# Kernel tuning notes

Measured on AMD Instinct MI355X. Metric: run time of the kernel, lower is better.

## Reference

```python
import jax, jax.numpy as jnp
import numpy as np

N_HEAD = 32
N_KV_HEAD = 8
HEAD_DIM = 64
ROPE_BASE = 10000.0


def _rope_tables(T, dim):
    inv_freq = 1.0 / (ROPE_BASE ** (jnp.arange(0, dim, 2, dtype=jnp.float32) / dim))
    t = jnp.arange(T, dtype=jnp.float32)
    freqs = jnp.outer(t, inv_freq)            # [T, dim/2]
    emb = jnp.concatenate([freqs, freqs], -1)  # [T, dim]
    return jnp.cos(emb), jnp.sin(emb)


def _rotate_half(x):
    x1, x2 = jnp.split(x, 2, axis=-1)
    return jnp.concatenate([-x2, x1], axis=-1)


def setup_inputs() -> dict:
    key = jax.random.key(0)
    ks = jax.random.split(key, 5)
    B, T, C = 2, 2048, 2048
    kv_dim = N_KV_HEAD * HEAD_DIM
    s = 0.02
    return {
        "x":  jax.random.normal(ks[0], (B, T, C), jnp.float32),
        "Wq": jax.random.normal(ks[1], (C, C), jnp.float32) * s,
        "Wk": jax.random.normal(ks[2], (C, kv_dim), jnp.float32) * s,
        "Wv": jax.random.normal(ks[3], (C, kv_dim), jnp.float32) * s,
        "Wo": jax.random.normal(ks[4], (C, C), jnp.float32) * s,
    }


def reference(x, Wq, Wk, Wv, Wo):
    B, T, C = x.shape
    n_rep = N_HEAD // N_KV_HEAD  # 4 query heads per KV head

    q = (x @ Wq).reshape(B, T, N_HEAD, HEAD_DIM).transpose(0, 2, 1, 3)      # [B,H,T,d]
    k = (x @ Wk).reshape(B, T, N_KV_HEAD, HEAD_DIM).transpose(0, 2, 1, 3)   # [B,Hk,T,d]
    v = (x @ Wv).reshape(B, T, N_KV_HEAD, HEAD_DIM).transpose(0, 2, 1, 3)   # [B,Hk,T,d]

    cos, sin = _rope_tables(T, HEAD_DIM)  # [T,d], broadcast over batch/heads
    q = q * cos + _rotate_half(q) * sin
    k = k * cos + _rotate_half(k) * sin

    # group Q heads by their shared KV head (equivalent to repeat_interleave on K/V)
    qg = q.reshape(B, N_KV_HEAD, n_rep, T, HEAD_DIM)
    scale = 1.0 / np.sqrt(HEAD_DIM).astype(np.float32)
    att = jnp.einsum('bgrtd,bgsd->bgrts', qg, k) * scale  # [B,Hk,rep,T,T]

    causal = jnp.tril(jnp.ones((T, T), dtype=bool))
    att = jnp.where(causal, att, -jnp.inf)
    att = jax.nn.softmax(att, axis=-1)

    y = jnp.einsum('bgrts,bgsd->bgrtd', att, v)            # [B,Hk,rep,T,d]
    y = y.reshape(B, N_HEAD, T, HEAD_DIM).transpose(0, 2, 1, 3).reshape(B, T, C)
    return y @ Wo
```

## Files before the change

### kernel.cpp

```cpp
#include <hip/hip_runtime.h>
#include <hip/hip_bf16.h>
#include <math.h>

#define B_SZ    2
#define T_SEQ   2048
#define C_DIM   2048
#define N_HEAD  32
#define N_KVH   8
#define HDIM    64
#define KV_DIM  (N_KVH * HDIM)
#define M_ROWS  (B_SZ * T_SEQ)
#define RLN     0.28782313662425575f

typedef __bf16 bf16x8 __attribute__((ext_vector_type(8)));
typedef float f32x4 __attribute__((ext_vector_type(4)));
typedef unsigned short u16x4 __attribute__((ext_vector_type(4)));
typedef unsigned short u16x8 __attribute__((ext_vector_type(8)));

__device__ inline unsigned short f2bf(float f) {
    __bf16 h = (__bf16)f;
    return __builtin_bit_cast(unsigned short, h);
}


__global__ __launch_bounds__(256) void convert_a(const float* __restrict__ A,
                                                 unsigned short* __restrict__ Ab,
                                                 int K) {
    const int G = blockIdx.x * 256 + threadIdx.x;
    const int t = G >> 10;
    const int w = G & 1023;
    const int g = w & 7, m = w >> 3;
    const int KT = K >> 6;
    const int mh = t / KT, kt = t % KT;
    const float* src = A + (size_t)(mh * 128 + m) * K + kt * 64 + g * 8;
    const float4 a = *(const float4*)src;
    const float4 b = *(const float4*)(src + 4);
    u16x8 o;
    o[0] = f2bf(a.x); o[1] = f2bf(a.y); o[2] = f2bf(a.z); o[3] = f2bf(a.w);
    o[4] = f2bf(b.x); o[5] = f2bf(b.y); o[6] = f2bf(b.z); o[7] = f2bf(b.w);
    *(u16x8*)(Ab + (size_t)t * 8192 + g * 1024 + m * 8) = o;
}

__global__ __launch_bounds__(256) void convert_w(const float* __restrict__ W,
                                                 unsigned short* __restrict__ Wb,
                                                 int K, int N) {
    const int G = blockIdx.x * 256 + threadIdx.x;
    const int t = G >> 10;
    const int w = G & 1023;
    const int n = w & 127, g = w >> 7;
    const int KT = K >> 6;
    const int nh = t / KT, kt = t % KT;
    const float* src = W + (size_t)(kt * 64 + g * 8) * N + nh * 128 + n;
    u16x8 o;
    #pragma unroll
    for (int j = 0; j < 8; ++j) o[j] = f2bf(src[(size_t)j * N]);
    *(u16x8*)(Wb + (size_t)t * 8192 + g * 1024 + n * 8) = o;
}

#define G_LDS16(SRC, DST)                                                      \
    __builtin_amdgcn_global_load_lds(                                          \
        (const __attribute__((address_space(1))) unsigned int*)(SRC),          \
        (__attribute__((address_space(3))) unsigned int*)(DST), 16, 0, 0)

#define STAGE(GB, LB)                                                          \
    do {                                                                       \
        G_LDS16((GB) + ch * 512 + lane * 8, (LB) + ch * 512);                  \
        G_LDS16((GB) + (ch + 1) * 512 + lane * 8, (LB) + (ch + 1) * 512);      \
    } while (0)

#define MFMA16(AF, IB, JB)                                                     \
    _Pragma("unroll")                                                          \
    for (int i_ = 0; i_ < 4; ++i_)                                             \
        _Pragma("unroll")                                                      \
        for (int j_ = 0; j_ < 2; ++j_) {                                       \
            acc[(IB) + i_][(JB) + j_] = __builtin_amdgcn_mfma_f32_16x16x32_bf16( \
                AF[i_][0], bfr[(JB) + j_][0], acc[(IB) + i_][(JB) + j_], 0, 0, 0); \
            acc[(IB) + i_][(JB) + j_] = __builtin_amdgcn_mfma_f32_16x16x32_bf16( \
                AF[i_][1], bfr[(JB) + j_][1], acc[(IB) + i_][(JB) + j_], 0, 0, 0); \
        }

__device__ __forceinline__ void gemm256_core(const unsigned short* __restrict__ Ab,
                                             const unsigned short* __restrict__ Bb,
                                             const int K, f32x4 (&acc)[8][4]) {
    __shared__ __align__(16) unsigned short lds[2][4][8192];

    const int tid  = threadIdx.x;
    const int wave = tid >> 6, lane = tid & 63;
    const int quad = lane >> 4, l15 = lane & 15;
    const int wm = wave >> 2, wn = wave & 3;
    const int NT = K >> 6;
    const unsigned short* At = Ab + (size_t)(blockIdx.y * 2) * NT * 8192;
    const unsigned short* Bt = Bb + (size_t)(blockIdx.x * 2) * NT * 8192;
    const int ch = wave * 2;

    const int abase = quad * 1024 + l15 * 8;
    const int bbase = quad * 1024 + ((wn & 1) * 64 + l15) * 8;

    #pragma unroll
    for (int i = 0; i < 8; ++i)
        #pragma unroll
        for (int j = 0; j < 4; ++j) acc[i][j] = (f32x4){0.f, 0.f, 0.f, 0.f};

    STAGE(At,                              lds[0][0]);
    STAGE(At + (size_t)NT * 8192,          lds[0][1]);
    STAGE(Bt,                              lds[0][2]);
    STAGE(Bt + (size_t)NT * 8192,          lds[0][3]);
    STAGE(At + 8192,                       lds[1][0]);
    STAGE(At + (size_t)NT * 8192 + 8192,   lds[1][1]);
    asm volatile("s_waitcnt vmcnt(4)" ::: "memory");
    __builtin_amdgcn_s_barrier();

    for (int t = 0; t < NT; ++t) {
        unsigned short (*L)[8192]  = lds[t & 1];
        unsigned short (*Ln)[8192] = lds[(t & 1) ^ 1];
        const unsigned short* Abuf = L[wm];
        const unsigned short* Bbuf = L[2 + (wn >> 1)];
        bf16x8 af0[4][2], af1[4][2], bfr[4][2];

        #pragma unroll
        for (int i = 0; i < 4; ++i) {
            af0[i][0] = *(const bf16x8*)(Abuf + abase + i * 128);
            af0[i][1] = *(const bf16x8*)(Abuf + abase + 4096 + i * 128);
        }
        #pragma unroll
        for (int j = 0; j < 2; ++j) {
            bfr[j][0] = *(const bf16x8*)(Bbuf + bbase + j * 128);
            bfr[j][1] = *(const bf16x8*)(Bbuf + bbase + 4096 + j * 128);
        }
        if (t + 1 < NT) STAGE(Bt + (size_t)(t + 1) * 8192, Ln[2]);
        asm volatile("s_waitcnt lgkmcnt(8)" ::: "memory");
        __builtin_amdgcn_s_barrier();
        asm volatile("s_waitcnt lgkmcnt(0)" ::: "memory");
        __builtin_amdgcn_sched_barrier(0);
        __builtin_amdgcn_s_setprio(1);
        MFMA16(af0, 0, 0)
        __builtin_amdgcn_s_setprio(0);
        __builtin_amdgcn_sched_barrier(0);
        __builtin_amdgcn_s_barrier();

        #pragma unroll
        for (int i = 0; i < 4; ++i) {
            af1[i][0] = *(const bf16x8*)(Abuf + abase + (4 + i) * 128);
            af1[i][1] = *(const bf16x8*)(Abuf + abase + 4096 + (4 + i) * 128);
        }
        #pragma unroll
        for (int j = 0; j < 2; ++j) {
            bfr[2 + j][0] = *(const bf16x8*)(Bbuf + bbase + (2 + j) * 128);
            bfr[2 + j][1] = *(const bf16x8*)(Bbuf + bbase + 4096 + (2 + j) * 128);
        }
        if (t + 1 < NT) STAGE(Bt + (size_t)(NT + t + 1) * 8192, Ln[3]);
        asm volatile("s_waitcnt lgkmcnt(8)" ::: "memory");
        __builtin_amdgcn_s_barrier();
        asm volatile("s_waitcnt lgkmcnt(0)" ::: "memory");
        __builtin_amdgcn_sched_barrier(0);
        __builtin_amdgcn_s_setprio(1);
        MFMA16(af1, 4, 0)
        __builtin_amdgcn_s_setprio(0);
        __builtin_amdgcn_sched_barrier(0);
        __builtin_amdgcn_s_barrier();

        if (t + 2 < NT) STAGE(At + (size_t)(t + 2) * 8192, L[0]);
        __builtin_amdgcn_s_barrier();
        __builtin_amdgcn_sched_barrier(0);
        __builtin_amdgcn_s_setprio(1);
        MFMA16(af0, 0, 2)
        __builtin_amdgcn_s_setprio(0);
        __builtin_amdgcn_sched_barrier(0);
        __builtin_amdgcn_s_barrier();

        if (t + 2 < NT) {
            STAGE(At + (size_t)(NT + t + 2) * 8192, L[1]);
            asm volatile("s_waitcnt vmcnt(4)" ::: "memory");
        } else {
            asm volatile("s_waitcnt vmcnt(0)" ::: "memory");
        }
        __builtin_amdgcn_s_barrier();
        __builtin_amdgcn_sched_barrier(0);
        __builtin_amdgcn_s_setprio(1);
        MFMA16(af1, 4, 2)
        __builtin_amdgcn_s_setprio(0);
        __builtin_amdgcn_sched_barrier(0);
        __builtin_amdgcn_s_barrier();
    }
}

__global__ __launch_bounds__(512, 2) void gemm256(const unsigned short* __restrict__ Ab,
                                                  const unsigned short* __restrict__ Bb,
                                                  float* __restrict__ C,
                                                  int N, int K) {
    f32x4 acc[8][4];
    gemm256_core(Ab, Bb, K, acc);
    const int tid  = threadIdx.x;
    const int wave = tid >> 6, lane = tid & 63;
    const int quad = lane >> 4, l15 = lane & 15;
    const int wm = wave >> 2, wn = wave & 3;
    const int row0 = blockIdx.y * 256 + wm * 128 + quad * 4;
    const int col0 = blockIdx.x * 256 + wn * 64 + l15;
    #pragma unroll
    for (int i = 0; i < 8; ++i)
        #pragma unroll
        for (int r = 0; r < 4; ++r) {
            const int row = row0 + i * 16 + r;
            #pragma unroll
            for (int j = 0; j < 4; ++j)
                C[(size_t)row * N + col0 + j * 16] = acc[i][j][r];
        }
}

__global__ __launch_bounds__(512, 2) void gemm256_qkv(const unsigned short* __restrict__ Ab,
                                                      const unsigned short* __restrict__ Bb,
                                                      unsigned short* __restrict__ Qb,
                                                      unsigned short* __restrict__ Kbuf,
                                                      unsigned short* __restrict__ Vt,
                                                      int K) {
    f32x4 acc[8][4];
    gemm256_core(Ab, Bb, K, acc);
    const int tid  = threadIdx.x;
    const int wave = tid >> 6, lane = tid & 63;
    const int quad = lane >> 4, l15 = lane & 15;
    const int wm = wave >> 2, wn = wave & 3;
    const int cb = blockIdx.x * 256 + wn * 64;
    const int m0 = blockIdx.y * 256 + wm * 128 + quad * 4;

    if (cb < 2048) {
        const int h = cb >> 6;
        const float invf0 = __expf(-(float)l15 * RLN);
        const float invf1 = __expf(-(float)(l15 + 16) * RLN);
        #pragma unroll
        for (int i = 0; i < 8; ++i)
            #pragma unroll
            for (int r = 0; r < 4; ++r) {
                const int row = m0 + i * 16 + r;
                const float t = (float)(row & (T_SEQ - 1));
                float s0, c0, s1, c1;
                sincosf(t * invf0, &s0, &c0);
                sincosf(t * invf1, &s1, &c1);
                const float x0 = acc[i][0][r], x1 = acc[i][1][r];
                const float x2 = acc[i][2][r], x3 = acc[i][3][r];
                unsigned short* dst = Qb + (size_t)row * C_DIM + h * HDIM + l15;
                dst[0]  = f2bf((x0 * c0 - x2 * s0) * 0.125f);
                dst[16] = f2bf((x1 * c1 - x3 * s1) * 0.125f);
                dst[32] = f2bf((x2 * c0 + x0 * s0) * 0.125f);
                dst[48] = f2bf((x3 * c1 + x1 * s1) * 0.125f);
            }
    } else if (cb < 2560) {
        const int kvh = (cb - 2048) >> 6;
        const float invf0 = __expf(-(float)l15 * RLN);
        const float invf1 = __expf(-(float)(l15 + 16) * RLN);
        const int c8l = l15 >> 3, dil = l15 & 7;
        #pragma unroll
        for (int i = 0; i < 8; ++i)
            #pragma unroll
            for (int r = 0; r < 4; ++r) {
                const int row = m0 + i * 16 + r;
                const int tt = row & (T_SEQ - 1);
                const int bb = row >> 11;
                const float t = (float)tt;
                float s0, c0, s1, c1;
                sincosf(t * invf0, &s0, &c0);
                sincosf(t * invf1, &s1, &c1);
                const float x0 = acc[i][0][r], x1 = acc[i][1][r];
                const float x2 = acc[i][2][r], x3 = acc[i][3][r];
                unsigned short* dst = Kbuf + (size_t)((bb * N_KVH + kvh) * 32 + (tt >> 6)) * 4096;
                const int kk = tt & 63;
                dst[((c8l + 0) * 64 + kk) * 8 + dil] = f2bf(x0 * c0 - x2 * s0);
                dst[((c8l + 2) * 64 + kk) * 8 + dil] = f2bf(x1 * c1 - x3 * s1);
                dst[((c8l + 4) * 64 + kk) * 8 + dil] = f2bf(x2 * c0 + x0 * s0);
                dst[((c8l + 6) * 64 + kk) * 8 + dil] = f2bf(x3 * c1 + x1 * s1);
            }
    } else {
        const int kvh = (cb - 2560) >> 6;
        const int bb = m0 >> 11;
        #pragma unroll
        for (int i = 0; i < 8; ++i) {
            const int t0 = (m0 + i * 16) & (T_SEQ - 1);
            const int o = (t0 >> 3) & 7, i8 = t0 & 7;
            unsigned short* dst = Vt + (size_t)((bb * N_KVH + kvh) * 32 + (t0 >> 6)) * 4096;
            #pragma unroll
            for (int j = 0; j < 4; ++j) {
                const int d = j * 16 + l15;
                u16x4 pk;
                pk[0] = f2bf(acc[i][j][0]); pk[1] = f2bf(acc[i][j][1]);
                pk[2] = f2bf(acc[i][j][2]); pk[3] = f2bf(acc[i][j][3]);
                *(u16x4*)(dst + (o * 64 + d) * 8 + i8) = pk;
            }
        }
    }
}

__global__ __launch_bounds__(256, 2) void attn_mfma(const unsigned short* __restrict__ Qb,
                                                    const unsigned short* __restrict__ Kbuf,
                                                    const unsigned short* __restrict__ Vt,
                                                    unsigned short* __restrict__ Yb) {
    __shared__ __align__(16) unsigned short Ps[4][1152];

    const int bid = blockIdx.x;
    const int x   = bid & 7;
    const int g   = bid >> 3;
    const int combo = x * 2 + (g & 1);
    const int qc  = 31 - (g >> 1);
    const int b   = combo >> 3;
    const int kvh = combo & 7;

    const int tid  = threadIdx.x;
    const int wave = tid >> 6, lane = tid & 63;
    const int quad = lane >> 4, l15 = lane & 15;
    const int h    = kvh * 4 + wave;
    const int qw   = qc * 64;

    bf16x8 qf[4][2];
    #pragma unroll
    for (int mt = 0; mt < 4; ++mt) {
        const size_t qoff = (size_t)(b * T_SEQ + qw + mt * 16 + l15) * C_DIM + h * HDIM + quad * 8;
        qf[mt][0] = *(const bf16x8*)(Qb + qoff);
        qf[mt][1] = *(const bf16x8*)(Qb + qoff + 32);
    }

    const unsigned short* kbase = Kbuf + (size_t)((b * N_KVH + kvh) * 32) * 4096;
    const unsigned short* vbase = Vt + (size_t)((b * N_KVH + kvh) * 32) * 4096;

    f32x4 acc[4][4];
    #pragma unroll
    for (int mt = 0; mt < 4; ++mt)
        #pragma unroll
        for (int c = 0; c < 4; ++c) acc[mt][c] = (f32x4){0.f, 0.f, 0.f, 0.f};
    float psum[4][4];
    #pragma unroll
    for (int mt = 0; mt < 4; ++mt)
        #pragma unroll
        for (int r = 0; r < 4; ++r) psum[mt][r] = 0.f;

    for (int jt = 0; jt <= qc; ++jt) {
        const unsigned short* kt = kbase + (size_t)jt * 4096;
        const unsigned short* vt = vbase + (size_t)jt * 4096;

        bf16x8 kf[4][2], vf[2][4];
        #pragma unroll
        for (int st = 0; st < 4; ++st)
            #pragma unroll
            for (int c = 0; c < 2; ++c)
                kf[st][c] = *(const bf16x8*)&kt[((c * 4 + quad) * 64 + l15 * 4 + st) * 8];
        #pragma unroll
        for (int kc = 0; kc < 2; ++kc)
            #pragma unroll
            for (int c = 0; c < 4; ++c)
                vf[kc][c] = *(const bf16x8*)&vt[((kc * 4 + quad) * 64 + c * 16 + l15) * 8];

        const bool diag = (jt == qc);
        const int j0 = jt << 6;

        #pragma unroll
        for (int mt = 0; mt < 4; ++mt) {
            f32x4 sacc[4];
            #pragma unroll
            for (int st = 0; st < 4; ++st) {
                f32x4 s = (f32x4){0.f, 0.f, 0.f, 0.f};
                s = __builtin_amdgcn_mfma_f32_16x16x32_bf16(qf[mt][0], kf[st][0], s, 0, 0, 0);
                s = __builtin_amdgcn_mfma_f32_16x16x32_bf16(qf[mt][1], kf[st][1], s, 0, 0, 0);
                sacc[st] = s;
            }

            float p[4][4];
            if (!diag) {
                #pragma unroll
                for (int st = 0; st < 4; ++st)
                    #pragma unroll
                    for (int r = 0; r < 4; ++r)
                        p[st][r] = __expf(sacc[st][r]);
            } else {
                #pragma unroll
                for (int st = 0; st < 4; ++st)
                    #pragma unroll
                    for (int r = 0; r < 4; ++r) {
                        const int key = j0 + l15 * 4 + st;
                        const int q   = qw + mt * 16 + quad * 4 + r;
                        p[st][r] = __expf(key > q ? -1e30f : sacc[st][r]);
                    }
            }
            #pragma unroll
            for (int r = 0; r < 4; ++r) {
                u16x4 pk;
                pk[0] = f2bf(p[0][r]); pk[1] = f2bf(p[1][r]);
                pk[2] = f2bf(p[2][r]); pk[3] = f2bf(p[3][r]);
                *(u16x4*)&Ps[wave][(quad * 4 + r) * 72 + l15 * 4] = pk;
                psum[mt][r] += (p[0][r] + p[1][r]) + (p[2][r] + p[3][r]);
            }

            #pragma unroll
            for (int kc = 0; kc < 2; ++kc) {
                const bf16x8 pa = *(const bf16x8*)&Ps[wave][l15 * 72 + kc * 32 + quad * 8];
                #pragma unroll
                for (int c = 0; c < 4; ++c)
                    acc[mt][c] = __builtin_amdgcn_mfma_f32_16x16x32_bf16(pa, vf[kc][c], acc[mt][c], 0, 0, 0);
            }
        }
    }

    #pragma unroll
    for (int mt = 0; mt < 4; ++mt)
        #pragma unroll
        for (int r = 0; r < 4; ++r) {
            float s = psum[mt][r];
            #pragma unroll
            for (int off = 1; off < 16; off <<= 1) s += __shfl_xor(s, off, 16);
            const float inv = 1.0f / s;
            const int grow = b * T_SEQ + qw + mt * 16 + quad * 4 + r;
            const int mh = grow >> 7, m = grow & 127;
            #pragma unroll
            for (int c = 0; c < 4; ++c) {
                const int gk = c * 2 + (l15 >> 3);
                Yb[(size_t)(mh * 32 + h) * 8192 + gk * 1024 + m * 8 + (l15 & 7)]
                    = f2bf(acc[mt][c][r] * inv);
            }
        }
}

extern "C" void kernel_launch(void* const* d_in, const int* in_sizes, int n_in,
                              void* d_out, int out_size, void* d_ws, size_t ws_size,
                              hipStream_t stream) {
    const float* x  = (const float*)d_in[0];
    const float* Wq = (const float*)d_in[1];
    const float* Wk = (const float*)d_in[2];
    const float* Wv = (const float*)d_in[3];
    const float* Wo = (const float*)d_in[4];

    char* base = (char*)d_ws;
    unsigned short* xb    = (unsigned short*)(base + 0);
    unsigned short* Wqkvb = (unsigned short*)(base + (16ull << 20));
    unsigned short* Wob   = (unsigned short*)(base + (28ull << 20));
    unsigned short* Qb    = (unsigned short*)(base + (36ull << 20));
    unsigned short* Kb    = (unsigned short*)(base + (52ull << 20));
    unsigned short* Vt    = (unsigned short*)(base + (56ull << 20));
    unsigned short* Yb    = xb;

    const dim3 blk(256);

    convert_a<<<(M_ROWS * C_DIM) / 2048, blk, 0, stream>>>(x, xb, C_DIM);
    convert_w<<<(C_DIM * C_DIM) / 2048, blk, 0, stream>>>(Wq, Wqkvb, C_DIM, C_DIM);
    convert_w<<<(C_DIM * KV_DIM) / 2048, blk, 0, stream>>>(Wk, Wqkvb + (size_t)16 * 32 * 8192, C_DIM, KV_DIM);
    convert_w<<<(C_DIM * KV_DIM) / 2048, blk, 0, stream>>>(Wv, Wqkvb + (size_t)20 * 32 * 8192, C_DIM, KV_DIM);
    convert_w<<<(C_DIM * C_DIM) / 2048, blk, 0, stream>>>(Wo, Wob, C_DIM, C_DIM);

    gemm256_qkv<<<dim3(3072 / 256, M_ROWS / 256), dim3(512), 0, stream>>>(xb, Wqkvb, Qb, Kb, Vt, C_DIM);

    attn_mfma<<<B_SZ * N_KVH * (T_SEQ / 64), blk, 0, stream>>>(Qb, Kb, Vt, Yb);

    gemm256<<<dim3(C_DIM / 256, M_ROWS / 256), dim3(512), 0, stream>>>(Yb, Wob, (float*)d_out, C_DIM, C_DIM);
}
```

Baseline: 331.2 us.

## Reorder GEMM phases to reuse A fragments and cut fragment registers

```diff
diff --git a/kernel.cpp b/kernel.cpp
--- a/kernel.cpp
+++ b/kernel.cpp
@@ -68,16 +68,41 @@
         G_LDS16((GB) + (ch + 1) * 512 + lane * 8, (LB) + (ch + 1) * 512);      \
     } while (0)
 
-#define MFMA16(AF, IB, JB)                                                     \
+#define MFMA16(IB, JB)                                                         \
     _Pragma("unroll")                                                          \
     for (int i_ = 0; i_ < 4; ++i_)                                             \
         _Pragma("unroll")                                                      \
         for (int j_ = 0; j_ < 2; ++j_) {                                       \
             acc[(IB) + i_][(JB) + j_] = __builtin_amdgcn_mfma_f32_16x16x32_bf16( \
-                AF[i_][0], bfr[(JB) + j_][0], acc[(IB) + i_][(JB) + j_], 0, 0, 0); \
+                af[i_][0], bf[j_][0], acc[(IB) + i_][(JB) + j_], 0, 0, 0);     \
             acc[(IB) + i_][(JB) + j_] = __builtin_amdgcn_mfma_f32_16x16x32_bf16( \
-                AF[i_][1], bfr[(JB) + j_][1], acc[(IB) + i_][(JB) + j_], 0, 0, 0); \
-        }
+                af[i_][1], bf[j_][1], acc[(IB) + i_][(JB) + j_], 0, 0, 0);     \
+        }
+
+#define READ_AF(ROW0)                                                          \
+    _Pragma("unroll")                                                          \
+    for (int i_ = 0; i_ < 4; ++i_) {                                           \
+        af[i_][0] = *(const bf16x8*)(Abuf + abase + ((ROW0) + i_) * 128);      \
+        af[i_][1] = *(const bf16x8*)(Abuf + abase + 4096 + ((ROW0) + i_) * 128); \
+    }
+
+#define READ_BF(COL0)                                                          \
+    _Pragma("unroll")                                                          \
+    for (int j_ = 0; j_ < 2; ++j_) {                                           \
+        bf[j_][0] = *(const bf16x8*)(Bbuf + bbase + ((COL0) + j_) * 128);      \
+        bf[j_][1] = *(const bf16x8*)(Bbuf + bbase + 4096 + ((COL0) + j_) * 128); \
+    }
+
+#define PHASE_TAIL()                                                           \
+    __builtin_amdgcn_s_barrier();                                              \
+    asm volatile("s_waitcnt lgkmcnt(0)" ::: "memory");                         \
+    __builtin_amdgcn_sched_barrier(0);                                         \
+    __builtin_amdgcn_s_setprio(1)
+
+#define PHASE_END()                                                            \
+    __builtin_amdgcn_s_setprio(0);                                             \
+    __builtin_amdgcn_sched_barrier(0);                                         \
+    __builtin_amdgcn_s_barrier()
 
 __device__ __forceinline__ void gemm256_core(const unsigned short* __restrict__ Ab,
                                              const unsigned short* __restrict__ Bb,
@@ -115,72 +140,40 @@
         unsigned short (*Ln)[8192] = lds[(t & 1) ^ 1];
         const unsigned short* Abuf = L[wm];
         const unsigned short* Bbuf = L[2 + (wn >> 1)];
-        bf16x8 af0[4][2], af1[4][2], bfr[4][2];
-
-        #pragma unroll
-        for (int i = 0; i < 4; ++i) {
-            af0[i][0] = *(const bf16x8*)(Abuf + abase + i * 128);
-            af0[i][1] = *(const bf16x8*)(Abuf + abase + 4096 + i * 128);
-        }
-        #pragma unroll
-        for (int j = 0; j < 2; ++j) {
-            bfr[j][0] = *(const bf16x8*)(Bbuf + bbase + j * 128);
-            bfr[j][1] = *(const bf16x8*)(Bbuf + bbase + 4096 + j * 128);
-        }
+        bf16x8 af[4][2], bf[2][2];
+
+        READ_AF(0)
+        READ_BF(0)
         if (t + 1 < NT) STAGE(Bt + (size_t)(t + 1) * 8192, Ln[2]);
         asm volatile("s_waitcnt lgkmcnt(8)" ::: "memory");
-        __builtin_amdgcn_s_barrier();
-        asm volatile("s_waitcnt lgkmcnt(0)" ::: "memory");
-        __builtin_amdgcn_sched_barrier(0);
-        __builtin_amdgcn_s_setprio(1);
-        MFMA16(af0, 0, 0)
-        __builtin_amdgcn_s_setprio(0);
-        __builtin_amdgcn_sched_barrier(0);
-        __builtin_amdgcn_s_barrier();
-
-        #pragma unroll
-        for (int i = 0; i < 4; ++i) {
-            af1[i][0] = *(const bf16x8*)(Abuf + abase + (4 + i) * 128);
-            af1[i][1] = *(const bf16x8*)(Abuf + abase + 4096 + (4 + i) * 128);
-        }
-        #pragma unroll
-        for (int j = 0; j < 2; ++j) {
-            bfr[2 + j][0] = *(const bf16x8*)(Bbuf + bbase + (2 + j) * 128);
-            bfr[2 + j][1] = *(const bf16x8*)(Bbuf + bbase + 4096 + (2 + j) * 128);
-        }
+        PHASE_TAIL();
+        MFMA16(0, 0)
+        PHASE_END();
+
+        READ_BF(2)
         if (t + 1 < NT) STAGE(Bt + (size_t)(NT + t + 1) * 8192, Ln[3]);
+        PHASE_TAIL();
+        MFMA16(0, 2)
+        PHASE_END();
+
+        READ_AF(4)
+        READ_BF(0)
         asm volatile("s_waitcnt lgkmcnt(8)" ::: "memory");
-        __builtin_amdgcn_s_barrier();
-        asm volatile("s_waitcnt lgkmcnt(0)" ::: "memory");
-        __builtin_amdgcn_sched_barrier(0);
-        __builtin_amdgcn_s_setprio(1);
-        MFMA16(af1, 4, 0)
-        __builtin_amdgcn_s_setprio(0);
-        __builtin_amdgcn_sched_barrier(0);
-        __builtin_amdgcn_s_barrier();
-
-        if (t + 2 < NT) STAGE(At + (size_t)(t + 2) * 8192, L[0]);
-        __builtin_amdgcn_s_barrier();
-        __builtin_amdgcn_sched_barrier(0);
-        __builtin_amdgcn_s_setprio(1);
-        MFMA16(af0, 0, 2)
-        __builtin_amdgcn_s_setprio(0);
-        __builtin_amdgcn_sched_barrier(0);
-        __builtin_amdgcn_s_barrier();
-
+        PHASE_TAIL();
+        MFMA16(4, 0)
+        PHASE_END();
+
+        READ_BF(2)
         if (t + 2 < NT) {
+            STAGE(At + (size_t)(t + 2) * 8192, L[0]);
             STAGE(At + (size_t)(NT + t + 2) * 8192, L[1]);
             asm volatile("s_waitcnt vmcnt(4)" ::: "memory");
         } else {
             asm volatile("s_waitcnt vmcnt(0)" ::: "memory");
         }
-        __builtin_amdgcn_s_barrier();
-        __builtin_amdgcn_sched_barrier(0);
-        __builtin_amdgcn_s_setprio(1);
-        MFMA16(af1, 4, 2)
-        __builtin_amdgcn_s_setprio(0);
-        __builtin_amdgcn_sched_barrier(0);
-        __builtin_amdgcn_s_barrier();
+        PHASE_TAIL();
+        MFMA16(4, 2)
+        PHASE_END();
     }
 }
 
```

New measurement: 338.2 us. +2.1%, slower.
